# Performance work log

Hardware: AMD Instinct MI355X
Metric: run time of the kernel (lower is better)

Reference implementation:

```python
import jax, jax.numpy as jnp
import numpy as np

BLOCK_SIZE = 256
N_EMBD = 768
HEAD_SIZE = 768  # == n_embd so RoPE table (dim=n_embd) matches channel pairing


def _rope_tables(T, dim, theta0=10000.0):
    # compute_freq(dim=n_embd, seq_len=block_size, theta_0=10000):
    # theta_j = theta0^(-2j/dim), angle[t, j] = t * theta_j
    j = jnp.arange(dim // 2, dtype=jnp.float32)
    theta = jnp.float32(theta0) ** (-2.0 * j / jnp.float32(dim))
    ang = jnp.arange(T, dtype=jnp.float32)[:, None] * theta[None, :]  # [T, dim/2]
    return jnp.cos(ang), jnp.sin(ang)


def _apply_rope(t, cos, sin):
    # t: [B, T, D]; pair adjacent channels (2j, 2j+1) as complex, rotate.
    B, T, D = t.shape
    tr = t.reshape(B, T, D // 2, 2)
    re, im = tr[..., 0], tr[..., 1]
    out_re = re * cos[None] - im * sin[None]
    out_im = re * sin[None] + im * cos[None]
    return jnp.stack([out_re, out_im], axis=-1).reshape(B, T, D)


def setup_inputs() -> dict:
    key = jax.random.key(0)
    k1, k2, k3, k4 = jax.random.split(key, 4)
    B, T = 128, BLOCK_SIZE
    x = jax.random.normal(k1, (B, T, N_EMBD), dtype=jnp.float32)
    Wq = jax.random.normal(k2, (N_EMBD, HEAD_SIZE), dtype=jnp.float32) * 0.02
    Wk = jax.random.normal(k3, (N_EMBD, HEAD_SIZE), dtype=jnp.float32) * 0.02
    Wv = jax.random.normal(k4, (N_EMBD, HEAD_SIZE), dtype=jnp.float32) * 0.02
    return {"x": x, "Wq": Wq, "Wk": Wk, "Wv": Wv}


def reference(x, Wq, Wk, Wv):
    B, T, C = x.shape
    q = x @ Wq  # [B, T, D]
    k = x @ Wk
    v = x @ Wv
    cos, sin = _rope_tables(T, HEAD_SIZE)
    q = _apply_rope(q, cos, sin)
    k = _apply_rope(k, cos, sin)
    scale = jnp.float32(HEAD_SIZE) ** -0.5
    wei = jnp.einsum('bqd,bkd->bqk', q, k) * scale  # [B, T, T]
    causal = jnp.tril(jnp.ones((T, T), dtype=bool))
    wei = jnp.where(causal[None], wei, -jnp.inf)
    wei = jax.nn.softmax(wei, axis=-1)
    # dropout(p=0.2) is identity in eval/deterministic baseline
    out = jnp.einsum('bqk,bkd->bqd', wei, v)  # [B, T, D]
    return out
```

## Files before the change

### kernel.cpp

```cpp
#include <hip/hip_runtime.h>
#include <hip/hip_bf16.h>
#include <stdint.h>


typedef __attribute__((ext_vector_type(8))) short short8;
typedef __attribute__((ext_vector_type(4))) short short4v;
typedef __attribute__((ext_vector_type(4))) float f32x4;

__device__ __forceinline__ short f2bf(float f) {
    uint32_t u = __float_as_uint(f);
    u += 0x7fffu + ((u >> 16) & 1u);
    return (short)(u >> 16);
}

__global__ __launch_bounds__(256) void cvt_x(const float* __restrict__ x,
                                             short* __restrict__ xb) {
    long i = ((long)blockIdx.x * 256 + threadIdx.x) * 4;
    f32x4 v = *(const f32x4*)(x + i);
    short4v o;
    o.x = f2bf(v.x); o.y = f2bf(v.y); o.z = f2bf(v.z); o.w = f2bf(v.w);
    *(short4v*)(xb + i) = o;
}

__global__ __launch_bounds__(256) void cvt_wt(const float* __restrict__ W,
                                              short* __restrict__ Wt) {
    __shared__ float tile[32][33];
    int d0 = blockIdx.x * 32, c0 = blockIdx.y * 32;
    int tr = threadIdx.x >> 5, tc = threadIdx.x & 31;
    #pragma unroll
    for (int i = 0; i < 32; i += 8)
        tile[tr + i][tc] = W[(long)(c0 + tr + i) * 768 + d0 + tc];
    __syncthreads();
    #pragma unroll
    for (int i = 0; i < 32; i += 8)
        Wt[(long)(d0 + tr + i) * 768 + c0 + tc] = f2bf(tile[tc][tr + i]);
}

__global__ __launch_bounds__(256) void rope_tab(float2* __restrict__ rt) {
    int i = blockIdx.x * 256 + threadIdx.x;
    int t = i / 384, j = i - t * 384;
    const float CE = -0.034603417655f;
    float th = exp2f((float)j * CE);
    float s, c;
    sincosf((float)t * th, &s, &c);
    rt[i] = make_float2(c, s);
}

__global__ __launch_bounds__(512, 2)
void qkv256(const short* __restrict__ A, const short* __restrict__ B,
            short* __restrict__ Q, short* __restrict__ Kb,
            short* __restrict__ Vt, const float2* __restrict__ rt) {
    int p = blockIdx.x;
    int c = p & 7, j = p >> 3;
    int st = j / 9;
    int bx = j - st * 9;
    int by = c * 16 + st;
    const int m0 = by * 256, n0 = bx * 256;

    __shared__ short lA[2][256 * 64];
    __shared__ short lB[2][256 * 64];

    const int tid = threadIdx.x;
    const int w = tid >> 6, lane = tid & 63;
    const int wm = (w >> 2) * 128;
    const int wn = (w & 3) * 64;
    const int lr8 = lane >> 3;
    const int scol = (((lane & 7) - lr8) & 7) * 8;
    const int fr = lane & 15, kq = lane >> 4;

    f32x4 acc[8][4] = {};
    short8 af[4][2];
    short8 bq[4][2];

#define STAGE_HALF(lX, gX, r0g, h, t) do {                                     \
    int _buf = (t) & 1;                                                        \
    _Pragma("unroll")                                                          \
    for (int _i = 0; _i < 2; ++_i) {                                           \
        int _rl = (h) * 128 + (w * 2 + _i) * 8;                                \
        const short* _g = (gX) + (long)((r0g) + _rl + lr8) * 768               \
                               + (t) * 64 + scol;                              \
        __builtin_amdgcn_global_load_lds(                                      \
            (const __attribute__((address_space(1))) void*)_g,                 \
            (__attribute__((address_space(3))) void*)(&lX[_buf][_rl * 64]),    \
            16, 0, 0);                                                         \
    }                                                                          \
} while (0)

#define LOAD_A(mh, buf) do {                                                   \
    _Pragma("unroll")                                                          \
    for (int _t = 0; _t < 4; ++_t)                                             \
        _Pragma("unroll")                                                      \
        for (int _k = 0; _k < 2; ++_k)                                         \
            af[_t][_k] = *(const short8*)(&lA[buf][                            \
                (wm + (mh) * 64 + _t * 16 + fr) * 64 +                         \
                ((_k * 4 + kq + fr) & 7) * 8]);                                \
} while (0)

#define LOAD_B(nh, buf) do {                                                   \
    _Pragma("unroll")                                                          \
    for (int _t = 0; _t < 2; ++_t)                                             \
        _Pragma("unroll")                                                      \
        for (int _k = 0; _k < 2; ++_k)                                         \
            bq[(nh) * 2 + _t][_k] = *(const short8*)(&lB[buf][                 \
                (wn + (nh) * 32 + _t * 16 + fr) * 64 +                         \
                ((_k * 4 + kq + fr) & 7) * 8]);                                \
} while (0)

#define MMA_Q(mh, nh) do {                                                     \
    __builtin_amdgcn_s_setprio(1);                                             \
    _Pragma("unroll")                                                          \
    for (int _t = 0; _t < 4; ++_t)                                             \
        _Pragma("unroll")                                                      \
        for (int _n = 0; _n < 2; ++_n)                                         \
            _Pragma("unroll")                                                  \
            for (int _k = 0; _k < 2; ++_k)                                     \
                acc[(mh) * 4 + _t][(nh) * 2 + _n] =                            \
                    __builtin_amdgcn_mfma_f32_16x16x32_bf16(                   \
                        af[_t][_k], bq[(nh) * 2 + _n][_k],                     \
                        acc[(mh) * 4 + _t][(nh) * 2 + _n], 0, 0, 0);           \
    __builtin_amdgcn_s_setprio(0);                                             \
} while (0)

#define BAR() __builtin_amdgcn_s_barrier()
#define LGKM0() asm volatile("s_waitcnt lgkmcnt(0)" ::: "memory")
#define VMC4() asm volatile("s_waitcnt vmcnt(4)" ::: "memory")
#define VMC0() asm volatile("s_waitcnt vmcnt(0)" ::: "memory")

    STAGE_HALF(lB, B, n0, 0, 0);
    STAGE_HALF(lB, B, n0, 1, 0);
    STAGE_HALF(lA, A, m0, 0, 0);
    STAGE_HALF(lA, A, m0, 1, 0);
    STAGE_HALF(lB, B, n0, 0, 1);
    STAGE_HALF(lB, B, n0, 1, 1);
    VMC4();
    BAR();

    #pragma unroll 1
    for (int i = 0; i < 6; ++i) {
        const int t0 = 2 * i;
        const bool more = (i < 5);
        LOAD_A(0, 0); LOAD_B(0, 0);
        STAGE_HALF(lA, A, m0, 0, t0 + 1);
        BAR(); LGKM0(); MMA_Q(0, 0); BAR();
        LOAD_B(1, 0);
        STAGE_HALF(lA, A, m0, 1, t0 + 1);
        BAR(); LGKM0(); MMA_Q(0, 1); BAR();
        LOAD_A(1, 0);
        if (more) STAGE_HALF(lB, B, n0, 0, t0 + 2);
        BAR(); LGKM0(); MMA_Q(1, 1); BAR();
        if (more) STAGE_HALF(lB, B, n0, 1, t0 + 2);
        BAR(); LGKM0(); MMA_Q(1, 0);
        if (more) { VMC4(); } else { VMC0(); }
        BAR();
        LOAD_A(0, 1); LOAD_B(0, 1);
        if (more) STAGE_HALF(lA, A, m0, 0, t0 + 2);
        BAR(); LGKM0(); MMA_Q(0, 0); BAR();
        LOAD_B(1, 1);
        if (more) STAGE_HALF(lA, A, m0, 1, t0 + 2);
        BAR(); LGKM0(); MMA_Q(0, 1); BAR();
        LOAD_A(1, 1);
        if (more) STAGE_HALF(lB, B, n0, 0, t0 + 3);
        BAR(); LGKM0(); MMA_Q(1, 1); BAR();
        if (more) STAGE_HALF(lB, B, n0, 1, t0 + 3);
        BAR(); LGKM0(); MMA_Q(1, 0);
        if (more) VMC4();
        BAR();
    }

    const int type = (bx >= 6) ? 2 : (bx >= 3 ? 1 : 0);
    const int nl0 = n0 - type * 768;
    const int r0 = wm + (lane >> 4) * 4;
    const int c0 = wn + (lane & 15);
    if (type < 2) {
        short* dst = (type == 0) ? Q : Kb;
        const int par = lane & 1;
        #pragma unroll
        for (int tmi = 0; tmi < 8; ++tmi)
            #pragma unroll
            for (int tni = 0; tni < 4; ++tni) {
                int col = nl0 + c0 + tni * 16;
                const float2* rtc = rt + (col >> 1);
                #pragma unroll
                for (int r = 0; r < 4; ++r) {
                    int row = m0 + r0 + tmi * 16 + r;
                    float val = acc[tmi][tni][r];
                    float pv = __shfl_xor(val, 1);
                    float2 cs = rtc[(row & 255) * 384];
                    float re = par ? pv : val;
                    float im = par ? val : pv;
                    float o = par ? (re * cs.y + im * cs.x)
                                  : (re * cs.x - im * cs.y);
                    dst[(long)row * 768 + col] = f2bf(o);
                }
            }
    } else {
        #pragma unroll
        for (int tmi = 0; tmi < 8; ++tmi)
            #pragma unroll
            for (int tni = 0; tni < 4; ++tni) {
                int col = nl0 + c0 + tni * 16;
                #pragma unroll
                for (int r = 0; r < 4; ++r) {
                    int row = m0 + r0 + tmi * 16 + r;
                    Vt[((long)(row >> 8) * 768 + col) * 256 + (row & 255)] =
                        f2bf(acc[tmi][tni][r]);
                }
            }
    }
#undef STAGE_HALF
#undef LOAD_A
#undef LOAD_B
#undef MMA_Q
#undef BAR
#undef LGKM0
#undef VMC4
#undef VMC0
}

#define BARA() __builtin_amdgcn_s_barrier()
#define VMW(n) asm volatile("s_waitcnt vmcnt(%0)" :: "n"(n) : "memory")
#define LBAR() do { asm volatile("s_waitcnt lgkmcnt(0)" ::: "memory");         \
                    __builtin_amdgcn_s_barrier(); } while (0)
#define GLL(g, l) __builtin_amdgcn_global_load_lds(                            \
        (const __attribute__((address_space(1))) void*)(g),                    \
        (__attribute__((address_space(3))) void*)(l), 16, 0, 0)
#define AQK_STAGE(t) do { int _b = (t) & 1;                                    \
    _Pragma("unroll")                                                          \
    for (int _i = 0; _i < 2; ++_i) { int _s = _i * 4 + w;                      \
        GLL(Ab + (long)(_s * 8 + lr8) * 768 + (t) * 64 + scol,                 \
            smem + _b * 4096 + _s * 512); }                                    \
    _Pragma("unroll")                                                          \
    for (int _i = 0; _i < 2 * NC; ++_i) { int _s = _i * 4 + w;                 \
        GLL(Bb + (long)(_s * 8 + lr8) * 768 + (t) * 64 + scol,                 \
            smem + 8192 + _b * 16384 + _s * 512); } } while (0)
#define AV_STAGE(dc, kc, vb) do {                                              \
    _Pragma("unroll")                                                          \
    for (int _i = 0; _i < 4; ++_i) { int _s = _i * 4 + w;                      \
        GLL(Vb + (long)((dc) * 128 + _s * 8 + lr8) * 256 + (kc) * 64 + scol,   \
            smem + 16384 + (vb) * 8192 + _s * 512); } } while (0)

template <int NC>
__device__ __forceinline__ void attn_body(
    int bz, int qh, const short* __restrict__ Ab, const short* __restrict__ Bb,
    const short* __restrict__ Vb, float* __restrict__ out, float scale,
    short* smem, int w, int lane) {
    const int lr8 = lane >> 3;
    const int scol = (((lane & 7) - lr8) & 7) * 8;
    const int fr = lane & 15, kq = lane >> 4;
    const int wNC = w * NC;

    f32x4 acc[4][NC] = {};

    AQK_STAGE(0);
    AQK_STAGE(1);
    VMW(2 + 2 * NC);
    BARA();
    #pragma unroll 1
    for (int t = 0; t < 12; ++t) {
        const short* la = smem + (t & 1) * 4096;
        const short* lb = smem + 8192 + (t & 1) * 16384;
        #pragma unroll
        for (int cc = 0; cc < 2; ++cc) {
            const int sp = ((cc * 4 + kq + fr) & 7) * 8;
            short8 afr[4];
            #pragma unroll
            for (int tmi = 0; tmi < 4; ++tmi)
                afr[tmi] = *(const short8*)(la + (tmi * 16 + fr) * 64 + sp);
            #pragma unroll
            for (int tni = 0; tni < NC; ++tni) {
                short8 bfr = *(const short8*)(
                    lb + ((wNC + tni) * 16 + fr) * 64 + sp);
                #pragma unroll
                for (int tmi = 0; tmi < 4; ++tmi)
                    acc[tmi][tni] = __builtin_amdgcn_mfma_f32_16x16x32_bf16(
                        afr[tmi], bfr, acc[tmi][tni], 0, 0, 0);
            }
        }
        BARA();
        if (t < 10) { AQK_STAGE(t + 2); VMW(2 + 2 * NC); }
        else if (t == 10) { VMW(0); }
        BARA();
    }

    AV_STAGE(0, 0, 0);
    AV_STAGE(1 / NC, 1 % NC, 1);

    const int r0 = kq * 4;
    float* redm = (float*)(smem + 32768);
    float* reds = redm + 256;

    float M[16];
    #pragma unroll
    for (int tmi = 0; tmi < 4; ++tmi)
        #pragma unroll
        for (int r = 0; r < 4; ++r) {
            int rowL = tmi * 16 + r0 + r;
            int tloc = qh * 64 + rowL;
            float m = -1e30f;
            #pragma unroll
            for (int tni = 0; tni < NC; ++tni) {
                int col = (wNC + tni) * 16 + fr;
                float v = (col <= tloc) ? acc[tmi][tni][r] * scale : -1e30f;
                acc[tmi][tni][r] = v;
                m = fmaxf(m, v);
            }
            m = fmaxf(m, __shfl_xor(m, 1));
            m = fmaxf(m, __shfl_xor(m, 2));
            m = fmaxf(m, __shfl_xor(m, 4));
            m = fmaxf(m, __shfl_xor(m, 8));
            M[tmi * 4 + r] = m;
        }
    if (fr == 0) {
        #pragma unroll
        for (int tmi = 0; tmi < 4; ++tmi)
            #pragma unroll
            for (int r = 0; r < 4; ++r)
                redm[(tmi * 16 + r0 + r) * 4 + w] = M[tmi * 4 + r];
    }
    LBAR();
    #pragma unroll
    for (int tmi = 0; tmi < 4; ++tmi)
        #pragma unroll
        for (int r = 0; r < 4; ++r) {
            f32x4 v = *(const f32x4*)(redm + (tmi * 16 + r0 + r) * 4);
            M[tmi * 4 + r] = fmaxf(fmaxf(v.x, v.y), fmaxf(v.z, v.w));
        }
    float Sm[16];
    #pragma unroll
    for (int tmi = 0; tmi < 4; ++tmi)
        #pragma unroll
        for (int r = 0; r < 4; ++r) {
            float mm = M[tmi * 4 + r];
            float s = 0.f;
            #pragma unroll
            for (int tni = 0; tni < NC; ++tni) {
                float e = __expf(acc[tmi][tni][r] - mm);
                acc[tmi][tni][r] = e;
                s += e;
            }
            s += __shfl_xor(s, 1);
            s += __shfl_xor(s, 2);
            s += __shfl_xor(s, 4);
            s += __shfl_xor(s, 8);
            Sm[tmi * 4 + r] = s;
        }
    if (fr == 0) {
        #pragma unroll
        for (int tmi = 0; tmi < 4; ++tmi)
            #pragma unroll
            for (int r = 0; r < 4; ++r)
                reds[(tmi * 16 + r0 + r) * 4 + w] = Sm[tmi * 4 + r];
    }
    LBAR();

    #pragma unroll
    for (int tmi = 0; tmi < 4; ++tmi)
        #pragma unroll
        for (int r = 0; r < 4; ++r) {
            int rowL = tmi * 16 + r0 + r;
            f32x4 sv = *(const f32x4*)(reds + rowL * 4);
            float inv = 1.0f / (sv.x + sv.y + sv.z + sv.w);
            #pragma unroll
            for (int tni = 0; tni < NC; ++tni) {
                int ct = wNC + tni;
                int l = (ct & 3) * 2 + (fr >> 3);
                smem[(ct >> 2) * 4096 + rowL * 64 +
                     ((l + rowL) & 7) * 8 + (fr & 7)] =
                    f2bf(acc[tmi][tni][r] * inv);
            }
        }
    asm volatile("s_waitcnt lgkmcnt(0)" ::: "memory");
    VMW(4);
    BARA();

    const long rowB = (long)bz * 256 + (long)qh * 64;
    int s = 0;
    #pragma unroll 1
    for (int dc = 0; dc < 6; ++dc) {
        f32x4 a2[4][2] = {};
        #pragma unroll 1
        for (int kc = 0; kc < NC; ++kc, ++s) {
            const short* pch = smem + kc * 4096;
            const short* lv = smem + 16384 + (s & 1) * 8192;
            #pragma unroll
            for (int cc = 0; cc < 2; ++cc) {
                const int sp = ((cc * 4 + kq + fr) & 7) * 8;
                short8 ap[4], bv[2];
                #pragma unroll
                for (int tmi = 0; tmi < 4; ++tmi)
                    ap[tmi] = *(const short8*)(pch + (tmi * 16 + fr) * 64 + sp);
                #pragma unroll
                for (int tn = 0; tn < 2; ++tn)
                    bv[tn] = *(const short8*)(lv + (w * 32 + tn * 16 + fr) * 64 + sp);
                #pragma unroll
                for (int tmi = 0; tmi < 4; ++tmi)
                    #pragma unroll
                    for (int tn = 0; tn < 2; ++tn)
                        a2[tmi][tn] = __builtin_amdgcn_mfma_f32_16x16x32_bf16(
                            ap[tmi], bv[tn], a2[tmi][tn], 0, 0, 0);
            }
            const bool stq = (kc == NC - 1);
            if (stq) {
                #pragma unroll
                for (int tmi = 0; tmi < 4; ++tmi)
                    #pragma unroll
                    for (int tn = 0; tn < 2; ++tn)
                        #pragma unroll
                        for (int r = 0; r < 4; ++r) {
                            long row = rowB + tmi * 16 + kq * 4 + r;
                            int col = dc * 128 + w * 32 + tn * 16 + fr;
                            out[row * 768 + col] = a2[tmi][tn][r];
                        }
            }
            BARA();
            const int s2 = s + 2;
            const bool pre = (s2 < 6 * NC);
            if (pre) AV_STAGE(s2 / NC, s2 % NC, s & 1);
            if (stq && pre)      VMW(36);
            else if (stq)        VMW(32);
            else if (pre)        VMW(4);
            else                 VMW(0);
            BARA();
        }
    }
}

__global__ __launch_bounds__(256)
void attn3(const short* __restrict__ Qm, const short* __restrict__ Km,
           const short* __restrict__ Vm, float* __restrict__ out,
           float scale) {
    __shared__ short smem[40960];
    int p = blockIdx.x;
    int c = p & 7, j = p >> 3;
    int b = j >> 2, q0 = j & 3;
    int qh = (b & 8) ? 3 - q0 : q0;
    int bz = c * 16 + b;
    const short* Ab = Qm + (long)bz * 196608 + (long)qh * 49152;
    const short* Bb = Km + (long)bz * 196608;
    const short* Vb = Vm + (long)bz * 196608;
    int w = threadIdx.x >> 6, lane = threadIdx.x & 63;
    switch (qh) {
        case 0:  attn_body<1>(bz, qh, Ab, Bb, Vb, out, scale, smem, w, lane); break;
        case 1:  attn_body<2>(bz, qh, Ab, Bb, Vb, out, scale, smem, w, lane); break;
        case 2:  attn_body<3>(bz, qh, Ab, Bb, Vb, out, scale, smem, w, lane); break;
        default: attn_body<4>(bz, qh, Ab, Bb, Vb, out, scale, smem, w, lane); break;
    }
}
#undef BARA
#undef VMW
#undef LBAR
#undef GLL
#undef AQK_STAGE
#undef AV_STAGE

extern "C" void kernel_launch(void* const* d_in, const int* in_sizes, int n_in,
                              void* d_out, int out_size, void* d_ws, size_t ws_size,
                              hipStream_t stream) {
    const float* x  = (const float*)d_in[0];
    const float* Wq = (const float*)d_in[1];
    const float* Wk = (const float*)d_in[2];
    const float* Wv = (const float*)d_in[3];

    char* ws = (char*)d_ws;
    short*  xb = (short*)(ws);
    short*  wt = (short*)(ws + 50331648);
    short*  qb = (short*)(ws + 53870592);
    short*  kb = (short*)(ws + 104202240);
    short*  vt = (short*)(ws + 154533888);
    float2* rt = (float2*)(ws + 255197184);

    cvt_x<<<24576, 256, 0, stream>>>(x, xb);
    dim3 gw(24, 24);
    cvt_wt<<<gw, 256, 0, stream>>>(Wq, wt);
    cvt_wt<<<gw, 256, 0, stream>>>(Wk, wt + 589824);
    cvt_wt<<<gw, 256, 0, stream>>>(Wv, wt + 1179648);
    rope_tab<<<384, 256, 0, stream>>>(rt);

    qkv256<<<1152, 512, 0, stream>>>(xb, wt, qb, kb, vt, rt);

    attn3<<<512, 256, 0, stream>>>(qb, kb, vt, (float*)d_out, 0.0360843918f);
}
```

Measured before the change: 412.6 us.

## Load attention Q/K/V operands directly into registers instead of LDS staging

The attention kernel no longer stages Q, K and V tiles through LDS with global_load_lds and double-buffered barriers. MFMA fragments are now loaded straight from global memory into registers using a two-deep register prefetch. This removes most of the shared memory, which is cut to about 34KB, and most of the barriers. The smaller LDS footprint lets the launch bounds ask for 3 blocks per CU, trading LDS reuse for higher occupancy. The risk is that uncoalesced short8 global loads of 16-byte rows, and K/V being re-read by each wave through L2 rather than shared, raise memory latency.

```diff
diff --git a/kernel.cpp b/kernel.cpp
--- a/kernel.cpp
+++ b/kernel.cpp
@@ -217,76 +217,59 @@
 #undef VMC0
 }
 
-#define BARA() __builtin_amdgcn_s_barrier()
-#define VMW(n) asm volatile("s_waitcnt vmcnt(%0)" :: "n"(n) : "memory")
 #define LBAR() do { asm volatile("s_waitcnt lgkmcnt(0)" ::: "memory");         \
                     __builtin_amdgcn_s_barrier(); } while (0)
-#define GLL(g, l) __builtin_amdgcn_global_load_lds(                            \
-        (const __attribute__((address_space(1))) void*)(g),                    \
-        (__attribute__((address_space(3))) void*)(l), 16, 0, 0)
-#define AQK_STAGE(t) do { int _b = (t) & 1;                                    \
-    _Pragma("unroll")                                                          \
-    for (int _i = 0; _i < 2; ++_i) { int _s = _i * 4 + w;                      \
-        GLL(Ab + (long)(_s * 8 + lr8) * 768 + (t) * 64 + scol,                 \
-            smem + _b * 4096 + _s * 512); }                                    \
-    _Pragma("unroll")                                                          \
-    for (int _i = 0; _i < 2 * NC; ++_i) { int _s = _i * 4 + w;                 \
-        GLL(Bb + (long)(_s * 8 + lr8) * 768 + (t) * 64 + scol,                 \
-            smem + 8192 + _b * 16384 + _s * 512); } } while (0)
-#define AV_STAGE(dc, kc, vb) do {                                              \
-    _Pragma("unroll")                                                          \
-    for (int _i = 0; _i < 4; ++_i) { int _s = _i * 4 + w;                      \
-        GLL(Vb + (long)((dc) * 128 + _s * 8 + lr8) * 256 + (kc) * 64 + scol,   \
-            smem + 16384 + (vb) * 8192 + _s * 512); } } while (0)
 
 template <int NC>
-__device__ __forceinline__ void attn_body(
-    int bz, int qh, const short* __restrict__ Ab, const short* __restrict__ Bb,
-    const short* __restrict__ Vb, float* __restrict__ out, float scale,
+__device__ __forceinline__ void attn_core(
+    int bz, int qh, const short* __restrict__ qb, const short* __restrict__ kb,
+    const short* __restrict__ vt, float* __restrict__ out, float scale,
     short* smem, int w, int lane) {
-    const int lr8 = lane >> 3;
-    const int scol = (((lane & 7) - lr8) & 7) * 8;
     const int fr = lane & 15, kq = lane >> 4;
     const int wNC = w * NC;
-
-    f32x4 acc[4][NC] = {};
-
-    AQK_STAGE(0);
-    AQK_STAGE(1);
-    VMW(2 + 2 * NC);
-    BARA();
+    const short* Aq = qb + ((long)bz * 256 + qh * 64) * 768;
+    const short* Bk = kb + (long)bz * 196608;
+    const short* Vv = vt + (long)bz * 196608;
+
+    f32x4 acc[4][NC];
+    #pragma unroll
+    for (int m = 0; m < 4; ++m)
+        #pragma unroll
+        for (int n = 0; n < NC; ++n) acc[m][n] = (f32x4){0.f, 0.f, 0.f, 0.f};
+
+    short8 a0[4], a1[4], b0[NC], b1[NC];
+
+#define LDQ(ab, bb, ks) do {                                                   \
+    _Pragma("unroll")                                                          \
+    for (int _m = 0; _m < 4; ++_m)                                             \
+        ab[_m] = *(const short8*)(Aq + (long)(_m * 16 + fr) * 768              \
+                                  + (ks) * 32 + kq * 8);                       \
+    _Pragma("unroll")                                                          \
+    for (int _n = 0; _n < NC; ++_n)                                            \
+        bb[_n] = *(const short8*)(Bk + (long)((wNC + _n) * 16 + fr) * 768      \
+                                  + (ks) * 32 + kq * 8);                       \
+} while (0)
+#define MMQ(ab, bb) do {                                                       \
+    _Pragma("unroll")                                                          \
+    for (int _m = 0; _m < 4; ++_m)                                             \
+        _Pragma("unroll")                                                      \
+        for (int _n = 0; _n < NC; ++_n)                                        \
+            acc[_m][_n] = __builtin_amdgcn_mfma_f32_16x16x32_bf16(             \
+                ab[_m], bb[_n], acc[_m][_n], 0, 0, 0);                         \
+} while (0)
+
+    LDQ(a0, b0, 0);
+    LDQ(a1, b1, 1);
     #pragma unroll 1
-    for (int t = 0; t < 12; ++t) {
-        const short* la = smem + (t & 1) * 4096;
-        const short* lb = smem + 8192 + (t & 1) * 16384;
-        #pragma unroll
-        for (int cc = 0; cc < 2; ++cc) {
-            const int sp = ((cc * 4 + kq + fr) & 7) * 8;
-            short8 afr[4];
-            #pragma unroll
-            for (int tmi = 0; tmi < 4; ++tmi)
-                afr[tmi] = *(const short8*)(la + (tmi * 16 + fr) * 64 + sp);
-            #pragma unroll
-            for (int tni = 0; tni < NC; ++tni) {
-                short8 bfr = *(const short8*)(
-                    lb + ((wNC + tni) * 16 + fr) * 64 + sp);
-                #pragma unroll
-                for (int tmi = 0; tmi < 4; ++tmi)
-                    acc[tmi][tni] = __builtin_amdgcn_mfma_f32_16x16x32_bf16(
-                        afr[tmi], bfr, acc[tmi][tni], 0, 0, 0);
-            }
-        }
-        BARA();
-        if (t < 10) { AQK_STAGE(t + 2); VMW(2 + 2 * NC); }
-        else if (t == 10) { VMW(0); }
-        BARA();
-    }
-
-    AV_STAGE(0, 0, 0);
-    AV_STAGE(1 / NC, 1 % NC, 1);
+    for (int ks = 0; ks < 24; ks += 2) {
+        MMQ(a0, b0);
+        if (ks < 22) LDQ(a0, b0, ks + 2);
+        MMQ(a1, b1);
+        if (ks < 22) LDQ(a1, b1, ks + 3);
+    }
 
     const int r0 = kq * 4;
-    float* redm = (float*)(smem + 32768);
+    float* redm = (float*)(smem + 16384);
     float* reds = redm + 256;
 
     float M[16];
@@ -353,6 +336,17 @@
     }
     LBAR();
 
+    short8 v0[2], v1[2];
+#define LDV(vb, s) do {                                                        \
+    int _dc = (s) / (2 * NC), _ts = (s) - _dc * 2 * NC;                        \
+    _Pragma("unroll")                                                          \
+    for (int _tn = 0; _tn < 2; ++_tn)                                          \
+        vb[_tn] = *(const short8*)(Vv +                                        \
+            (long)(_dc * 128 + w * 32 + _tn * 16 + fr) * 256                   \
+            + _ts * 32 + kq * 8);                                              \
+} while (0)
+    LDV(v0, 0);
+
     #pragma unroll
     for (int tmi = 0; tmi < 4; ++tmi)
         #pragma unroll
@@ -369,89 +363,77 @@
                     f2bf(acc[tmi][tni][r] * inv);
             }
         }
-    asm volatile("s_waitcnt lgkmcnt(0)" ::: "memory");
-    VMW(4);
-    BARA();
-
+    LBAR();
+
+    f32x4 a2[4][2] = {};
     const long rowB = (long)bz * 256 + (long)qh * 64;
-    int s = 0;
+#define MMP(vb, s) do {                                                        \
+    int _dc2 = (s) / (2 * NC), _ts2 = (s) - _dc2 * 2 * NC;                     \
+    int _kc = _ts2 >> 1, _cc = _ts2 & 1;                                       \
+    const short* _p = smem + _kc * 4096;                                       \
+    const int _sp = ((_cc * 4 + kq + fr) & 7) * 8;                             \
+    _Pragma("unroll")                                                          \
+    for (int _m = 0; _m < 4; ++_m) {                                           \
+        short8 _ap = *(const short8*)(_p + (_m * 16 + fr) * 64 + _sp);         \
+        _Pragma("unroll")                                                      \
+        for (int _tn = 0; _tn < 2; ++_tn)                                      \
+            a2[_m][_tn] = __builtin_amdgcn_mfma_f32_16x16x32_bf16(             \
+                _ap, vb[_tn], a2[_m][_tn], 0, 0, 0);                           \
+    }                                                                          \
+} while (0)
+#define STO(dcv) do {                                                          \
+    _Pragma("unroll")                                                          \
+    for (int _m = 0; _m < 4; ++_m)                                             \
+        _Pragma("unroll")                                                      \
+        for (int _tn = 0; _tn < 2; ++_tn)                                      \
+            _Pragma("unroll")                                                  \
+            for (int _r = 0; _r < 4; ++_r) {                                   \
+                long _row = rowB + _m * 16 + kq * 4 + _r;                      \
+                int _col = (dcv) * 128 + w * 32 + _tn * 16 + fr;               \
+                out[_row * 768 + _col] = a2[_m][_tn][_r];                      \
+            }                                                                  \
+    _Pragma("unroll")                                                          \
+    for (int _m = 0; _m < 4; ++_m)                                             \
+        _Pragma("unroll")                                                      \
+        for (int _tn = 0; _tn < 2; ++_tn)                                      \
+            a2[_m][_tn] = (f32x4){0.f, 0.f, 0.f, 0.f};                         \
+} while (0)
+
+    LDV(v1, 1);
     #pragma unroll 1
-    for (int dc = 0; dc < 6; ++dc) {
-        f32x4 a2[4][2] = {};
-        #pragma unroll 1
-        for (int kc = 0; kc < NC; ++kc, ++s) {
-            const short* pch = smem + kc * 4096;
-            const short* lv = smem + 16384 + (s & 1) * 8192;
-            #pragma unroll
-            for (int cc = 0; cc < 2; ++cc) {
-                const int sp = ((cc * 4 + kq + fr) & 7) * 8;
-                short8 ap[4], bv[2];
-                #pragma unroll
-                for (int tmi = 0; tmi < 4; ++tmi)
-                    ap[tmi] = *(const short8*)(pch + (tmi * 16 + fr) * 64 + sp);
-                #pragma unroll
-                for (int tn = 0; tn < 2; ++tn)
-                    bv[tn] = *(const short8*)(lv + (w * 32 + tn * 16 + fr) * 64 + sp);
-                #pragma unroll
-                for (int tmi = 0; tmi < 4; ++tmi)
-                    #pragma unroll
-                    for (int tn = 0; tn < 2; ++tn)
-                        a2[tmi][tn] = __builtin_amdgcn_mfma_f32_16x16x32_bf16(
-                            ap[tmi], bv[tn], a2[tmi][tn], 0, 0, 0);
-            }
-            const bool stq = (kc == NC - 1);
-            if (stq) {
-                #pragma unroll
-                for (int tmi = 0; tmi < 4; ++tmi)
-                    #pragma unroll
-                    for (int tn = 0; tn < 2; ++tn)
-                        #pragma unroll
-                        for (int r = 0; r < 4; ++r) {
-                            long row = rowB + tmi * 16 + kq * 4 + r;
-                            int col = dc * 128 + w * 32 + tn * 16 + fr;
-                            out[row * 768 + col] = a2[tmi][tn][r];
-                        }
-            }
-            BARA();
-            const int s2 = s + 2;
-            const bool pre = (s2 < 6 * NC);
-            if (pre) AV_STAGE(s2 / NC, s2 % NC, s & 1);
-            if (stq && pre)      VMW(36);
-            else if (stq)        VMW(32);
-            else if (pre)        VMW(4);
-            else                 VMW(0);
-            BARA();
-        }
-    }
-}
-
-__global__ __launch_bounds__(256)
-void attn3(const short* __restrict__ Qm, const short* __restrict__ Km,
+    for (int s = 0; s < 12 * NC; s += 2) {
+        MMP(v0, s);
+        if (s + 2 < 12 * NC) LDV(v0, s + 2);
+        MMP(v1, s + 1);
+        if (s + 3 < 12 * NC) LDV(v1, s + 3);
+        if (((s + 2) % (2 * NC)) == 0) STO((s + 1) / (2 * NC));
+    }
+#undef LDQ
+#undef MMQ
+#undef LDV
+#undef MMP
+#undef STO
+}
+
+__global__ __launch_bounds__(256, 3)
+void attn4(const short* __restrict__ Qm, const short* __restrict__ Km,
            const short* __restrict__ Vm, float* __restrict__ out,
            float scale) {
-    __shared__ short smem[40960];
+    __shared__ short smem[17408];
     int p = blockIdx.x;
     int c = p & 7, j = p >> 3;
     int b = j >> 2, q0 = j & 3;
     int qh = (b & 8) ? 3 - q0 : q0;
     int bz = c * 16 + b;
-    const short* Ab = Qm + (long)bz * 196608 + (long)qh * 49152;
-    const short* Bb = Km + (long)bz * 196608;
-    const short* Vb = Vm + (long)bz * 196608;
     int w = threadIdx.x >> 6, lane = threadIdx.x & 63;
     switch (qh) {
-        case 0:  attn_body<1>(bz, qh, Ab, Bb, Vb, out, scale, smem, w, lane); break;
-        case 1:  attn_body<2>(bz, qh, Ab, Bb, Vb, out, scale, smem, w, lane); break;
-        case 2:  attn_body<3>(bz, qh, Ab, Bb, Vb, out, scale, smem, w, lane); break;
-        default: attn_body<4>(bz, qh, Ab, Bb, Vb, out, scale, smem, w, lane); break;
-    }
-}
-#undef BARA
-#undef VMW
+        case 0:  attn_core<1>(bz, qh, Qm, Km, Vm, out, scale, smem, w, lane); break;
+        case 1:  attn_core<2>(bz, qh, Qm, Km, Vm, out, scale, smem, w, lane); break;
+        case 2:  attn_core<3>(bz, qh, Qm, Km, Vm, out, scale, smem, w, lane); break;
+        default: attn_core<4>(bz, qh, Qm, Km, Vm, out, scale, smem, w, lane); break;
+    }
+}
 #undef LBAR
-#undef GLL
-#undef AQK_STAGE
-#undef AV_STAGE
 
 extern "C" void kernel_launch(void* const* d_in, const int* in_sizes, int n_in,
                               void* d_out, int out_size, void* d_ws, size_t ws_size,
@@ -478,5 +460,5 @@
 
     qkv256<<<1152, 512, 0, stream>>>(xb, wt, qb, kb, vt, rt);
 
-    attn3<<<512, 256, 0, stream>>>(qb, kb, vt, (float*)d_out, 0.0360843918f);
-}
+    attn4<<<512, 256, 0, stream>>>(qb, kb, vt, (float*)d_out, 0.0360843918f);
+}
```

Result: no change. 410.7 us (-0.5%).
